# Kernel tuning notes

Hardware: AMD Instinct MI355X
Metric: run time of the kernel (lower is better)

## Reference

```python
import jax, jax.numpy as jnp
import numpy as np

# ---- config (matches init_kwargs) ----
SPATIAL_SCALE = 0.0625
POOLED = 7
OUT_DIM = 256
SAMPLE_PER_PART = 4
TRANS_STD = 0.1
PART_SIZE = 7
DEFORM_FC_DIM = 1024
# group_size == 1 -> position-sensitive group index is always 0, channel c == ctop


def _deform_roi_pool(feat, rois, offset, no_trans):
    """Faithful JAX port of DeformablePSROIPoolForward (DCNv2), group_size=1.
    feat: (B,C,H,W), rois: (N,5)=[b,x1,y1,x2,y2], offset: (N,2,P,P) or None.
    Returns (N,C,P,P)."""
    B, C, H, W = feat.shape
    N = rois.shape[0]
    P, S = POOLED, SAMPLE_PER_PART
    dt = feat.dtype
    featT = jnp.transpose(feat, (0, 2, 3, 1))  # (B,H,W,C) for spatial gathers

    b = rois[:, 0].astype(jnp.int32)
    rsw = jnp.round(rois[:, 1]) * SPATIAL_SCALE - 0.5
    rsh = jnp.round(rois[:, 2]) * SPATIAL_SCALE - 0.5
    rew = (jnp.round(rois[:, 3]) + 1.0) * SPATIAL_SCALE - 0.5
    reh = (jnp.round(rois[:, 4]) + 1.0) * SPATIAL_SCALE - 0.5
    roi_w = jnp.maximum(rew - rsw, 0.1)
    roi_h = jnp.maximum(reh - rsh, 0.1)
    bin_h = roi_h / P            # (N,)
    bin_w = roi_w / P
    sub_h = bin_h / S
    sub_w = bin_w / S

    ph = jnp.arange(P)
    pw = jnp.arange(P)
    part_h = jnp.floor(ph.astype(dt) / P * PART_SIZE).astype(jnp.int32)  # == ph when part_size==P
    part_w = jnp.floor(pw.astype(dt) / P * PART_SIZE).astype(jnp.int32)

    if no_trans:
        tx = jnp.zeros((N, P, P), dt)
        ty = jnp.zeros((N, P, P), dt)
    else:
        tx = offset[:, 0][:, part_h][:, :, part_w] * TRANS_STD  # (N,P,P)
        ty = offset[:, 1][:, part_h][:, :, part_w] * TRANS_STD

    hstart = ph.astype(dt)[None, :, None] * bin_h[:, None, None] + rsh[:, None, None] + ty * roi_h[:, None, None]
    wstart = pw.astype(dt)[None, None, :] * bin_w[:, None, None] + rsw[:, None, None] + tx * roi_w[:, None, None]

    ih = jnp.arange(S).astype(dt)
    iw = jnp.arange(S).astype(dt)
    # sample coords, shape (N,P,P,S,S); ih along axis -2, iw along axis -1
    h = hstart[..., None, None] + ih[:, None] * sub_h[:, None, None, None, None]
    w = wstart[..., None, None] + iw[None, :] * sub_w[:, None, None, None, None]

    valid = (w >= -0.5) & (w <= W - 0.5) & (h >= -0.5) & (h <= H - 0.5)
    hc = jnp.clip(h, 0.0, H - 1.0)
    wc = jnp.clip(w, 0.0, W - 1.0)
    h0 = jnp.floor(hc).astype(jnp.int32)
    w0 = jnp.floor(wc).astype(jnp.int32)
    h1 = jnp.minimum(h0 + 1, H - 1)
    w1 = jnp.minimum(w0 + 1, W - 1)
    lh = hc - h0.astype(dt)
    lw = wc - w0.astype(dt)

    bidx = b[:, None, None, None, None]

    def g(yy, xx):  # (N,P,P,S,S,C)
        return featT[bidx, yy, xx]

    val = (g(h0, w0) * ((1 - lh) * (1 - lw))[..., None]
           + g(h0, w1) * ((1 - lh) * lw)[..., None]
           + g(h1, w0) * (lh * (1 - lw))[..., None]
           + g(h1, w1) * (lh * lw)[..., None])
    val = jnp.where(valid[..., None], val, jnp.zeros((), dt))
    ssum = val.sum(axis=(3, 4))                       # (N,P,P,C)
    cnt = valid.sum(axis=(3, 4)).astype(dt)           # (N,P,P)
    out = jnp.where(cnt[..., None] > 0, ssum / jnp.maximum(cnt, 1.0)[..., None], jnp.zeros((), dt))
    return jnp.transpose(out, (0, 3, 1, 2))           # (N,C,P,P)


def setup_inputs() -> dict:
    key = jax.random.key(0)
    ks = jax.random.split(key, 12)
    B, C, H, W = 2, OUT_DIM, 100, 100
    N = 512
    img = H / SPATIAL_SCALE  # 1600

    feat = jax.random.normal(ks[0], (B, C, H, W), jnp.float32)

    bi = jax.random.randint(ks[1], (N,), 0, B).astype(jnp.float32)
    x1 = jax.random.uniform(ks[2], (N,), jnp.float32, 0.0, img - 420.0)
    y1 = jax.random.uniform(ks[3], (N,), jnp.float32, 0.0, img - 420.0)
    x2 = x1 + jax.random.uniform(ks[4], (N,), jnp.float32, 32.0, 400.0)
    y2 = y1 + jax.random.uniform(ks[5], (N,), jnp.float32, 32.0, 400.0)
    rois = jnp.stack([bi, x1, y1, x2, y2], axis=1)

    fin = POOLED * POOLED * OUT_DIM  # 12544
    w1 = jax.random.normal(ks[6], (DEFORM_FC_DIM, fin), jnp.float32) / np.sqrt(fin)
    b1 = jnp.zeros((DEFORM_FC_DIM,), jnp.float32)
    w2 = jax.random.normal(ks[7], (DEFORM_FC_DIM, DEFORM_FC_DIM), jnp.float32) / np.sqrt(DEFORM_FC_DIM)
    b2 = jnp.zeros((DEFORM_FC_DIM,), jnp.float32)
    # original init zeroes the last layer; use small random so offsets/mask are non-trivial
    w3 = jax.random.normal(ks[8], (POOLED * POOLED * 3, DEFORM_FC_DIM), jnp.float32) * 0.01
    b3 = jnp.zeros((POOLED * POOLED * 3,), jnp.float32)
    return {"input": feat, "rois": rois, "w1": w1, "b1": b1, "w2": w2, "b2": b2, "w3": w3, "b3": b3}


def reference(input, rois, w1, b1, w2, b2, w3, b3):
    N = rois.shape[0]
    P = POOLED
    # pass 1: plain (no_trans) deformable RoI pooling to predict offsets/mask
    roi0 = _deform_roi_pool(input, rois, None, no_trans=True)      # (N,C,P,P)
    x = roi0.reshape(N, -1)
    x = jax.nn.relu(x @ w1.T + b1)
    x = jax.nn.relu(x @ w2.T + b2)
    om = (x @ w3.T + b3).reshape(N, 3, P, P)
    offset = om[:, 0:2]                                            # (N,2,P,P) [trans_x, trans_y]
    mask = jax.nn.sigmoid(om[:, 2:3])                              # (N,1,P,P)
    # pass 2: deformable pooling with learned offsets, modulated by mask
    out = _deform_roi_pool(input, rois, offset, no_trans=False) * mask
    return out
```

## Files before the change

kernel.cpp:

```cpp
#include <hip/hip_runtime.h>

#define BB 2
#define CC 256
#define HH 100
#define WW 100
#define NROI 512
#define KDIM 12544
#define FC 1024

typedef _Float16 half_t;
typedef _Float16 f16x2 __attribute__((ext_vector_type(2)));
typedef _Float16 f16x8 __attribute__((ext_vector_type(8)));
typedef _Float16 f16x4 __attribute__((ext_vector_type(4)));
typedef float f32x4 __attribute__((ext_vector_type(4)));

__device__ __forceinline__ void gload16(const half_t* g, half_t* l) {
  __builtin_amdgcn_global_load_lds(
      (const __attribute__((address_space(1))) unsigned int*)g,
      (__attribute__((address_space(3))) unsigned int*)l, 16, 0, 0);
}

__global__ __launch_bounds__(256) void prep(const float* __restrict__ feat,
                                            half_t* __restrict__ featT,
                                            const float* __restrict__ w1,
                                            half_t* __restrict__ w1h,
                                            const float* __restrict__ w2,
                                            half_t* __restrict__ w2h) {
  int bid = blockIdx.x;
  if (bid < 12544) {
    int i4 = (bid * 256 + threadIdx.x) * 4;
    float4 v = *(const float4*)(w1 + i4);
    f16x4 o;
    o[0] = (half_t)v.x; o[1] = (half_t)v.y; o[2] = (half_t)v.z; o[3] = (half_t)v.w;
    *(f16x4*)(w1h + i4) = o;
    return;
  }
  bid -= 12544;
  if (bid < 1024) {
    int i4 = (bid * 256 + threadIdx.x) * 4;
    float4 v = *(const float4*)(w2 + i4);
    f16x4 o;
    o[0] = (half_t)v.x; o[1] = (half_t)v.y; o[2] = (half_t)v.z; o[3] = (half_t)v.w;
    *(f16x4*)(w2h + i4) = o;
    return;
  }
  bid -= 1024;
  __shared__ float tile[32][33];
  const int bx = bid % 313;
  const int rem = bid / 313;
  const int by = rem & 7;
  const int bz = rem >> 3;
  const int tx = threadIdx.x & 31, ty = threadIdx.x >> 5;
  const int hw0 = bx * 32;
  const int c0 = by * 32;
  const float* fb = feat + (size_t)bz * CC * (HH * WW);
#pragma unroll
  for (int i = 0; i < 4; i++) {
    int c = c0 + ty + i * 8;
    int hw = hw0 + tx;
    tile[ty + i * 8][tx] = (hw < HH * WW) ? fb[(size_t)c * (HH * WW) + hw] : 0.0f;
  }
  __syncthreads();
  half_t* ob = featT + (size_t)bz * (HH * WW) * CC;
#pragma unroll
  for (int i = 0; i < 4; i++) {
    int hw = hw0 + ty + i * 8;
    int c = c0 + tx;
    if (hw < HH * WW) ob[(size_t)hw * CC + c] = (half_t)tile[tx][ty + i * 8];
  }
}

struct PixW { int idx; float w; };

template <bool PASS2>
__global__ __launch_bounds__(512) void pool_kernel(const half_t* __restrict__ featT,
                                                   const float* __restrict__ rois,
                                                   const float* __restrict__ part3,
                                                   const float* __restrict__ b3,
                                                   half_t* __restrict__ xout,
                                                   float* __restrict__ out) {
  __shared__ __align__(16) PixW s_pix[49 * 32];
  __shared__ int s_cnt[49];
  __shared__ float s_scale[49];
  __shared__ float  s_outf[PASS2 ? KDIM : 1];
  __shared__ half_t s_outh[PASS2 ? 1 : KDIM];

  const int n = blockIdx.x;
  const int tid = threadIdx.x;
  const float* r = rois + n * 5;
  const int b = (int)r[0];
  const float rsw = rintf(r[1]) * 0.0625f - 0.5f;
  const float rsh = rintf(r[2]) * 0.0625f - 0.5f;
  const float rew = (rintf(r[3]) + 1.0f) * 0.0625f - 0.5f;
  const float reh = (rintf(r[4]) + 1.0f) * 0.0625f - 0.5f;
  const float roi_w = fmaxf(rew - rsw, 0.1f);
  const float roi_h = fmaxf(reh - rsh, 0.1f);
  const float bin_h = roi_h / 7.0f, bin_w = roi_w / 7.0f;
  const float sub_h = bin_h * 0.25f, sub_w = bin_w * 0.25f;
  const half_t* fb = featT + (size_t)b * (HH * WW) * CC;

  if (tid < 49) {
    const int p = tid, ph = p / 7, pw = p - ph * 7;
    float tx = 0.0f, ty = 0.0f, mask = 1.0f;
    if (PASS2) {
      float o0 = b3[p], o1 = b3[49 + p], o2 = b3[98 + p];
#pragma unroll
      for (int zz = 0; zz < 8; zz++) {
        const float* pz = part3 + ((size_t)zz * NROI + n) * 147;
        o0 += pz[p]; o1 += pz[49 + p]; o2 += pz[98 + p];
      }
      tx = o0 * 0.1f;
      ty = o1 * 0.1f;
      mask = 1.0f / (1.0f + expf(-o2));
    }
    const float hst = (float)ph * bin_h + rsh + ty * roi_h;
    const float wst = (float)pw * bin_w + rsw + tx * roi_w;
    float wh[6] = {0, 0, 0, 0, 0, 0};
    float hc0 = fminf(fmaxf(hst, 0.0f), 99.0f);
    const int r0 = (int)hc0;
    int rtop = r0;
    float vsh = 0.0f;
#pragma unroll
    for (int i = 0; i < 4; i++) {
      float h = hst + (float)i * sub_h;
      bool v = (h >= -0.5f) && (h <= (float)HH - 0.5f);
      float hc = fminf(fmaxf(h, 0.0f), 99.0f);
      int h0 = (int)hc;
      float lh = hc - (float)h0;
      int h1 = min(h0 + 1, HH - 1);
      if (v) { wh[h0 - r0] += 1.0f - lh; wh[h1 - r0] += lh; vsh += 1.0f; }
      rtop = h1;
    }
    float wwc[6] = {0, 0, 0, 0, 0, 0};
    float wc0 = fminf(fmaxf(wst, 0.0f), 99.0f);
    const int c0 = (int)wc0;
    int ctop = c0;
    float vsw = 0.0f;
#pragma unroll
    for (int j = 0; j < 4; j++) {
      float w = wst + (float)j * sub_w;
      bool v = (w >= -0.5f) && (w <= (float)WW - 0.5f);
      float wc = fminf(fmaxf(w, 0.0f), 99.0f);
      int w0 = (int)wc;
      float lw = wc - (float)w0;
      int w1 = min(w0 + 1, WW - 1);
      if (v) { wwc[w0 - c0] += 1.0f - lw; wwc[w1 - c0] += lw; vsw += 1.0f; }
      ctop = w1;
    }
    const int nr = rtop - r0 + 1, nc = ctop - c0 + 1;
    float cntf = vsh * vsw;
    s_scale[p] = (cntf > 0.0f) ? mask / cntf : 0.0f;
    PixW* dst = &s_pix[p * 32];
    int m = 0;
    for (int ri = 0; ri < nr; ri++) {
      int rowoff = (r0 + ri) * WW + c0;
      for (int ci = 0; ci < nc; ci++) {
        dst[m].idx = (rowoff + ci) * CC;
        dst[m].w = wh[ri] * wwc[ci];
        m++;
      }
    }
    while (m & 7) { dst[m].idx = 0; dst[m].w = 0.0f; m++; }
    s_cnt[p] = m;
  }
  __syncthreads();

  const int wv = tid >> 6;
  const int lane = tid & 63;
  const int half = lane >> 5;
  const int c8 = (lane & 31) * 8;
  for (int p = wv; p < 49; p += 8) {
    const int cnt = s_cnt[p];
    const PixW* cp = &s_pix[p * 32];
    float a0 = 0, a1 = 0, a2 = 0, a3 = 0, a4 = 0, a5 = 0, a6 = 0, a7 = 0;
    for (int q = 0; q < cnt; q += 8) {
      PixW e0 = cp[q + 0 + half];
      PixW e1 = cp[q + 2 + half];
      PixW e2 = cp[q + 4 + half];
      PixW e3 = cp[q + 6 + half];
      f16x8 v0 = *(const f16x8*)(fb + e0.idx + c8);
      f16x8 v1 = *(const f16x8*)(fb + e1.idx + c8);
      f16x8 v2 = *(const f16x8*)(fb + e2.idx + c8);
      f16x8 v3 = *(const f16x8*)(fb + e3.idx + c8);
      a0 += e0.w * (float)v0[0] + e1.w * (float)v1[0] + e2.w * (float)v2[0] + e3.w * (float)v3[0];
      a1 += e0.w * (float)v0[1] + e1.w * (float)v1[1] + e2.w * (float)v2[1] + e3.w * (float)v3[1];
      a2 += e0.w * (float)v0[2] + e1.w * (float)v1[2] + e2.w * (float)v2[2] + e3.w * (float)v3[2];
      a3 += e0.w * (float)v0[3] + e1.w * (float)v1[3] + e2.w * (float)v2[3] + e3.w * (float)v3[3];
      a4 += e0.w * (float)v0[4] + e1.w * (float)v1[4] + e2.w * (float)v2[4] + e3.w * (float)v3[4];
      a5 += e0.w * (float)v0[5] + e1.w * (float)v1[5] + e2.w * (float)v2[5] + e3.w * (float)v3[5];
      a6 += e0.w * (float)v0[6] + e1.w * (float)v1[6] + e2.w * (float)v2[6] + e3.w * (float)v3[6];
      a7 += e0.w * (float)v0[7] + e1.w * (float)v1[7] + e2.w * (float)v2[7] + e3.w * (float)v3[7];
    }
    a0 += __shfl_xor(a0, 32); a1 += __shfl_xor(a1, 32);
    a2 += __shfl_xor(a2, 32); a3 += __shfl_xor(a3, 32);
    a4 += __shfl_xor(a4, 32); a5 += __shfl_xor(a5, 32);
    a6 += __shfl_xor(a6, 32); a7 += __shfl_xor(a7, 32);
    if (half == 0) {
      float sc = s_scale[p];
      a0 *= sc; a1 *= sc; a2 *= sc; a3 *= sc; a4 *= sc; a5 *= sc; a6 *= sc; a7 *= sc;
      if (PASS2) {
        s_outf[(c8 + 0) * 49 + p] = a0;
        s_outf[(c8 + 1) * 49 + p] = a1;
        s_outf[(c8 + 2) * 49 + p] = a2;
        s_outf[(c8 + 3) * 49 + p] = a3;
        s_outf[(c8 + 4) * 49 + p] = a4;
        s_outf[(c8 + 5) * 49 + p] = a5;
        s_outf[(c8 + 6) * 49 + p] = a6;
        s_outf[(c8 + 7) * 49 + p] = a7;
      } else {
        s_outh[(c8 + 0) * 49 + p] = (half_t)a0;
        s_outh[(c8 + 1) * 49 + p] = (half_t)a1;
        s_outh[(c8 + 2) * 49 + p] = (half_t)a2;
        s_outh[(c8 + 3) * 49 + p] = (half_t)a3;
        s_outh[(c8 + 4) * 49 + p] = (half_t)a4;
        s_outh[(c8 + 5) * 49 + p] = (half_t)a5;
        s_outh[(c8 + 6) * 49 + p] = (half_t)a6;
        s_outh[(c8 + 7) * 49 + p] = (half_t)a7;
      }
    }
  }
  __syncthreads();

  if (PASS2) {
    float* ob = out + (size_t)n * KDIM;
    for (int l = tid * 4; l < KDIM; l += 2048)
      *(float4*)(ob + l) = *(const float4*)(s_outf + l);
  } else {
    half_t* ob = xout + (size_t)n * KDIM;
    for (int l = tid * 8; l < KDIM; l += 4096)
      *(f16x8*)(ob + l) = *(const f16x8*)(s_outh + l);
  }
}

template <int SK>
__global__ __launch_bounds__(256, 2) void gemm_lds(const half_t* __restrict__ A,
                                                   const half_t* __restrict__ B,
                                                   float* __restrict__ P, int K) {
  __shared__ half_t As[2][128 * 64];
  __shared__ half_t Bs[2][128 * 64];
  const int d = blockIdx.x + gridDim.x * (blockIdx.y + gridDim.y * blockIdx.z);
  const int g = (d & 7) * (SK * 4) + (d >> 3);
  const int z = g >> 5;
  const int tile = g & 31;
  const int m0 = (tile & 3) * 128;
  const int n0 = (tile >> 2) * 128;
  const int Kc = K / SK;
  const int kbeg = z * Kc;
  const int tid = threadIdx.x;
  const int lane = tid & 63;
  const int wave = tid >> 6;
  const int wm = (wave & 1) * 64;
  const int wn = (wave >> 1) * 64;
  const int fr = lane & 15;
  const int kc0 = lane >> 4;
  const int lr = lane >> 3;
  const int lc = (lane & 7) ^ lr;
  const half_t* Ag = A + (size_t)(m0 + wave * 8 + lr) * K + kbeg + lc * 8;
  const half_t* Bg = B + (size_t)(n0 + wave * 8 + lr) * K + kbeg + lc * 8;
  f32x4 acc[4][4] = {};

  auto stage = [&](int buf, int ko) {
#pragma unroll
    for (int s = 0; s < 4; s++)
      gload16(Ag + (size_t)(32 * s) * K + ko, &As[buf][s * 2048 + wave * 512]);
#pragma unroll
    for (int s = 0; s < 4; s++)
      gload16(Bg + (size_t)(32 * s) * K + ko, &Bs[buf][s * 2048 + wave * 512]);
  };

  const int iters = Kc >> 6;
  stage(0, 0);
  if (iters > 1) {
    stage(1, 64);
    asm volatile("s_waitcnt vmcnt(8)" ::: "memory");
  } else {
    asm volatile("s_waitcnt vmcnt(0)" ::: "memory");
  }
  __builtin_amdgcn_s_barrier();

  for (int it = 0; it < iters; it++) {
    const int cur = it & 1;
#pragma unroll
    for (int ks = 0; ks < 2; ks++) {
      const int swz = ((kc0 + ks * 4) ^ (fr & 7)) * 8;
      f16x8 af[4], bf[4];
#pragma unroll
      for (int i = 0; i < 4; i++) af[i] = *(const f16x8*)&As[cur][(wm + i * 16 + fr) * 64 + swz];
#pragma unroll
      for (int j = 0; j < 4; j++) bf[j] = *(const f16x8*)&Bs[cur][(wn + j * 16 + fr) * 64 + swz];
      __builtin_amdgcn_s_setprio(1);
#pragma unroll
      for (int i = 0; i < 4; i++)
#pragma unroll
        for (int j = 0; j < 4; j++)
          acc[i][j] = __builtin_amdgcn_mfma_f32_16x16x32_f16(af[i], bf[j], acc[i][j], 0, 0, 0);
      __builtin_amdgcn_s_setprio(0);
    }
    asm volatile("s_waitcnt lgkmcnt(0)" ::: "memory");
    __builtin_amdgcn_s_barrier();
    const bool issue = (it + 2 < iters);
    if (issue) stage(cur, (it + 2) * 64);
    if (it + 1 < iters) {
      if (issue) asm volatile("s_waitcnt vmcnt(8)" ::: "memory");
      else       asm volatile("s_waitcnt vmcnt(0)" ::: "memory");
      __builtin_amdgcn_s_barrier();
    }
  }
  float* Pz = P + (((size_t)z * 32 + tile) * 4 + wave) * 4096;
#pragma unroll
  for (int i = 0; i < 4; i++)
#pragma unroll
    for (int j = 0; j < 4; j++)
#pragma unroll
      for (int rr = 0; rr < 4; rr++)
        Pz[((i * 4 + j) * 4 + rr) * 64 + lane] = acc[i][j][rr];
}

template <bool OUT16, bool RELU, int SK>
__global__ __launch_bounds__(256) void reduce_blocked(const float* __restrict__ P,
                                                      const float* __restrict__ bias,
                                                      void* __restrict__ out,
                                                      int MN, int N) {
  int i4 = (blockIdx.x * 256 + threadIdx.x) * 4;
  if (i4 >= MN) return;
  float4 s = *(const float4*)(P + i4);
#pragma unroll
  for (int z = 1; z < SK; z++) {
    float4 t = *(const float4*)(P + (size_t)z * MN + i4);
    s.x += t.x; s.y += t.y; s.z += t.z; s.w += t.w;
  }
  const int lane0 = i4 & 63;
  const int q     = (i4 >> 6) & 63;
  const int wave  = (i4 >> 12) & 3;
  const int bx    = (i4 >> 14) & 3;
  const int by    = (i4 >> 16) & 7;
  const int rr = q & 3, j_ = (q >> 2) & 3, i_ = q >> 4;
  const int row = bx * 128 + (wave & 1) * 64 + i_ * 16 + (lane0 >> 4) * 4 + rr;
  const int col = by * 128 + (wave >> 1) * 64 + j_ * 16 + (lane0 & 15);
  float4 bv = *(const float4*)(bias + col);
  s.x += bv.x; s.y += bv.y; s.z += bv.z; s.w += bv.w;
  if (RELU) {
    s.x = fmaxf(s.x, 0.0f); s.y = fmaxf(s.y, 0.0f);
    s.z = fmaxf(s.z, 0.0f); s.w = fmaxf(s.w, 0.0f);
  }
  size_t o = (size_t)row * N + col;
  if (OUT16) {
    f16x4 ov;
    ov[0] = (half_t)s.x; ov[1] = (half_t)s.y; ov[2] = (half_t)s.z; ov[3] = (half_t)s.w;
    *(f16x4*)((half_t*)out + o) = ov;
  } else {
    *(float4*)((float*)out + o) = s;
  }
}

__global__ __launch_bounds__(192) void gemm3_part(const float* __restrict__ h2,
                                                  const float* __restrict__ w3,
                                                  float* __restrict__ part3) {
  __shared__ float hs[8][128];
  const int n0 = blockIdx.x * 8;
  const int z = blockIdx.y;
  const int tid = threadIdx.x;
  for (int idx = tid; idx < 1024; idx += 192) {
    int nn = idx >> 7, kk = idx & 127;
    hs[nn][kk] = h2[(size_t)(n0 + nn) * FC + z * 128 + kk];
  }
  __syncthreads();
  const int j = tid;
  if (j < 147) {
    const float* wr = w3 + (size_t)j * FC + z * 128;
    float acc[8] = {0, 0, 0, 0, 0, 0, 0, 0};
    for (int k = 0; k < 128; k += 4) {
      float4 wv = *(const float4*)(wr + k);
#pragma unroll
      for (int nn = 0; nn < 8; nn++)
        acc[nn] += hs[nn][k] * wv.x + hs[nn][k + 1] * wv.y +
                   hs[nn][k + 2] * wv.z + hs[nn][k + 3] * wv.w;
    }
#pragma unroll
    for (int nn = 0; nn < 8; nn++)
      part3[((size_t)z * NROI + n0 + nn) * 147 + j] = acc[nn];
  }
}

extern "C" void kernel_launch(void* const* d_in, const int* in_sizes, int n_in,
                              void* d_out, int out_size, void* d_ws, size_t ws_size,
                              hipStream_t stream) {
  const float* feat = (const float*)d_in[0];
  const float* rois = (const float*)d_in[1];
  const float* w1 = (const float*)d_in[2];
  const float* b1 = (const float*)d_in[3];
  const float* w2 = (const float*)d_in[4];
  const float* b2 = (const float*)d_in[5];
  const float* w3 = (const float*)d_in[6];
  const float* b3 = (const float*)d_in[7];
  float* out = (float*)d_out;
  char* ws = (char*)d_ws;

  half_t* featT = (half_t*)ws;
  half_t* xh    = (half_t*)(ws + 10240000);
  half_t* w1h   = (half_t*)(ws + 23085056);
  half_t* w2h   = (half_t*)(ws + 48775168);
  half_t* h1    = (half_t*)(ws + 50872320);
  float*  h2    = (float*)(ws + 51920896);
  float*  part  = (float*)(ws + 54319104);

  const int MN = NROI * FC;

  prep<<<dim3(18576), dim3(256), 0, stream>>>(feat, featT, w1, w1h, w2, w2h);
  pool_kernel<false><<<dim3(NROI), dim3(512), 0, stream>>>(featT, rois, nullptr, nullptr, xh, nullptr);

  gemm_lds<14><<<dim3(4, 8, 14), dim3(256), 0, stream>>>(xh, w1h, part, KDIM);
  reduce_blocked<true, true, 14><<<dim3(MN / 1024), dim3(256), 0, stream>>>(part, b1, (void*)h1, MN, FC);

  gemm_lds<8><<<dim3(4, 8, 8), dim3(256), 0, stream>>>(h1, w2h, part, FC);
  reduce_blocked<false, true, 8><<<dim3(MN / 1024), dim3(256), 0, stream>>>(part, b2, (void*)h2, MN, FC);

  gemm3_part<<<dim3(64, 8), dim3(192), 0, stream>>>(h2, w3, part);
  pool_kernel<true><<<dim3(NROI), dim3(512), 0, stream>>>(featT, rois, part, b3, nullptr, out);
}
```

Measured before the change: 220.3 us.

## Widen GEMM1 tiles, fuse GEMM2 reduce into GEMM3, unroll pooling gathers

GEMM1 moves to a 512-thread kernel with 256x128 tiles, which halves the tile count and reuses each B tile across more rows; its reduce kernel gets a matching index map. The separate GEMM2 split-K reduce is removed: the third GEMM now sums the eight partial slices, adds the bias and applies ReLU while loading its input tile. The pooling gather loop is unrolled to 16 entries, with padding raised to 16, so more loads are in flight. The cost is fewer blocks per GEMM1 wave, extra zero-weight padding gathers, and more register pressure.

```diff
diff --git a/kernel.cpp b/kernel.cpp
--- a/kernel.cpp
+++ b/kernel.cpp
@@ -160,7 +160,7 @@
         m++;
       }
     }
-    while (m & 7) { dst[m].idx = 0; dst[m].w = 0.0f; m++; }
+    while (m & 15) { dst[m].idx = 0; dst[m].w = 0.0f; m++; }
     s_cnt[p] = m;
   }
   __syncthreads();
@@ -173,23 +173,39 @@
     const int cnt = s_cnt[p];
     const PixW* cp = &s_pix[p * 32];
     float a0 = 0, a1 = 0, a2 = 0, a3 = 0, a4 = 0, a5 = 0, a6 = 0, a7 = 0;
-    for (int q = 0; q < cnt; q += 8) {
+    for (int q = 0; q < cnt; q += 16) {
       PixW e0 = cp[q + 0 + half];
       PixW e1 = cp[q + 2 + half];
       PixW e2 = cp[q + 4 + half];
       PixW e3 = cp[q + 6 + half];
+      PixW e4 = cp[q + 8 + half];
+      PixW e5 = cp[q + 10 + half];
+      PixW e6 = cp[q + 12 + half];
+      PixW e7 = cp[q + 14 + half];
       f16x8 v0 = *(const f16x8*)(fb + e0.idx + c8);
       f16x8 v1 = *(const f16x8*)(fb + e1.idx + c8);
       f16x8 v2 = *(const f16x8*)(fb + e2.idx + c8);
       f16x8 v3 = *(const f16x8*)(fb + e3.idx + c8);
-      a0 += e0.w * (float)v0[0] + e1.w * (float)v1[0] + e2.w * (float)v2[0] + e3.w * (float)v3[0];
-      a1 += e0.w * (float)v0[1] + e1.w * (float)v1[1] + e2.w * (float)v2[1] + e3.w * (float)v3[1];
-      a2 += e0.w * (float)v0[2] + e1.w * (float)v1[2] + e2.w * (float)v2[2] + e3.w * (float)v3[2];
-      a3 += e0.w * (float)v0[3] + e1.w * (float)v1[3] + e2.w * (float)v2[3] + e3.w * (float)v3[3];
-      a4 += e0.w * (float)v0[4] + e1.w * (float)v1[4] + e2.w * (float)v2[4] + e3.w * (float)v3[4];
-      a5 += e0.w * (float)v0[5] + e1.w * (float)v1[5] + e2.w * (float)v2[5] + e3.w * (float)v3[5];
-      a6 += e0.w * (float)v0[6] + e1.w * (float)v1[6] + e2.w * (float)v2[6] + e3.w * (float)v3[6];
-      a7 += e0.w * (float)v0[7] + e1.w * (float)v1[7] + e2.w * (float)v2[7] + e3.w * (float)v3[7];
+      f16x8 v4 = *(const f16x8*)(fb + e4.idx + c8);
+      f16x8 v5 = *(const f16x8*)(fb + e5.idx + c8);
+      f16x8 v6 = *(const f16x8*)(fb + e6.idx + c8);
+      f16x8 v7 = *(const f16x8*)(fb + e7.idx + c8);
+      a0 += e0.w * (float)v0[0] + e1.w * (float)v1[0] + e2.w * (float)v2[0] + e3.w * (float)v3[0]
+          + e4.w * (float)v4[0] + e5.w * (float)v5[0] + e6.w * (float)v6[0] + e7.w * (float)v7[0];
+      a1 += e0.w * (float)v0[1] + e1.w * (float)v1[1] + e2.w * (float)v2[1] + e3.w * (float)v3[1]
+          + e4.w * (float)v4[1] + e5.w * (float)v5[1] + e6.w * (float)v6[1] + e7.w * (float)v7[1];
+      a2 += e0.w * (float)v0[2] + e1.w * (float)v1[2] + e2.w * (float)v2[2] + e3.w * (float)v3[2]
+          + e4.w * (float)v4[2] + e5.w * (float)v5[2] + e6.w * (float)v6[2] + e7.w * (float)v7[2];
+      a3 += e0.w * (float)v0[3] + e1.w * (float)v1[3] + e2.w * (float)v2[3] + e3.w * (float)v3[3]
+          + e4.w * (float)v4[3] + e5.w * (float)v5[3] + e6.w * (float)v6[3] + e7.w * (float)v7[3];
+      a4 += e0.w * (float)v0[4] + e1.w * (float)v1[4] + e2.w * (float)v2[4] + e3.w * (float)v3[4]
+          + e4.w * (float)v4[4] + e5.w * (float)v5[4] + e6.w * (float)v6[4] + e7.w * (float)v7[4];
+      a5 += e0.w * (float)v0[5] + e1.w * (float)v1[5] + e2.w * (float)v2[5] + e3.w * (float)v3[5]
+          + e4.w * (float)v4[5] + e5.w * (float)v5[5] + e6.w * (float)v6[5] + e7.w * (float)v7[5];
+      a6 += e0.w * (float)v0[6] + e1.w * (float)v1[6] + e2.w * (float)v2[6] + e3.w * (float)v3[6]
+          + e4.w * (float)v4[6] + e5.w * (float)v5[6] + e6.w * (float)v6[6] + e7.w * (float)v7[6];
+      a7 += e0.w * (float)v0[7] + e1.w * (float)v1[7] + e2.w * (float)v2[7] + e3.w * (float)v3[7]
+          + e4.w * (float)v4[7] + e5.w * (float)v5[7] + e6.w * (float)v6[7] + e7.w * (float)v7[7];
     }
     a0 += __shfl_xor(a0, 32); a1 += __shfl_xor(a1, 32);
     a2 += __shfl_xor(a2, 32); a3 += __shfl_xor(a3, 32);
@@ -233,6 +249,126 @@
 }
 
 template <int SK>
+__global__ __launch_bounds__(512, 1) void gemm_lds_w(const half_t* __restrict__ A,
+                                                     const half_t* __restrict__ B,
+                                                     float* __restrict__ P, int K) {
+  __shared__ half_t As[2][256 * 64];
+  __shared__ half_t Bs[2][128 * 64];
+  const int d = blockIdx.x + gridDim.x * (blockIdx.y + gridDim.y * blockIdx.z);
+  const int g = (d & 7) * (SK * 2) + (d >> 3);
+  const int z = g >> 4;
+  const int tile = g & 15;
+  const int m0 = (tile & 1) * 256;
+  const int n0 = (tile >> 1) * 128;
+  const int Kc = K / SK;
+  const int kbeg = z * Kc;
+  const int tid = threadIdx.x;
+  const int lane = tid & 63;
+  const int wave = tid >> 6;
+  const int wm = (wave & 3) * 64;
+  const int wn = (wave >> 2) * 64;
+  const int fr = lane & 15;
+  const int kc0 = lane >> 4;
+  const int lr = lane >> 3;
+  const int lc = (lane & 7) ^ lr;
+  const half_t* Ag = A + (size_t)(m0 + wave * 32 + lr) * K + kbeg + lc * 8;
+  const half_t* Bg = B + (size_t)(n0 + wave * 16 + lr) * K + kbeg + lc * 8;
+  f32x4 acc[4][4] = {};
+
+  auto stage = [&](int buf, int ko) {
+#pragma unroll
+    for (int s = 0; s < 4; s++)
+      gload16(Ag + (size_t)(8 * s) * K + ko, &As[buf][wave * 2048 + s * 512]);
+#pragma unroll
+    for (int s = 0; s < 2; s++)
+      gload16(Bg + (size_t)(8 * s) * K + ko, &Bs[buf][wave * 1024 + s * 512]);
+  };
+
+  const int iters = Kc >> 6;
+  stage(0, 0);
+  if (iters > 1) {
+    stage(1, 64);
+    asm volatile("s_waitcnt vmcnt(6)" ::: "memory");
+  } else {
+    asm volatile("s_waitcnt vmcnt(0)" ::: "memory");
+  }
+  __builtin_amdgcn_s_barrier();
+
+  for (int it = 0; it < iters; it++) {
+    const int cur = it & 1;
+#pragma unroll
+    for (int ks = 0; ks < 2; ks++) {
+      const int swz = ((kc0 + ks * 4) ^ (fr & 7)) * 8;
+      f16x8 af[4], bf[4];
+#pragma unroll
+      for (int i = 0; i < 4; i++) af[i] = *(const f16x8*)&As[cur][(wm + i * 16 + fr) * 64 + swz];
+#pragma unroll
+      for (int j = 0; j < 4; j++) bf[j] = *(const f16x8*)&Bs[cur][(wn + j * 16 + fr) * 64 + swz];
+      __builtin_amdgcn_s_setprio(1);
+#pragma unroll
+      for (int i = 0; i < 4; i++)
+#pragma unroll
+        for (int j = 0; j < 4; j++)
+          acc[i][j] = __builtin_amdgcn_mfma_f32_16x16x32_f16(af[i], bf[j], acc[i][j], 0, 0, 0);
+      __builtin_amdgcn_s_setprio(0);
+    }
+    asm volatile("s_waitcnt lgkmcnt(0)" ::: "memory");
+    __builtin_amdgcn_s_barrier();
+    const bool issue = (it + 2 < iters);
+    if (issue) stage(cur, (it + 2) * 64);
+    if (it + 1 < iters) {
+      if (issue) asm volatile("s_waitcnt vmcnt(6)" ::: "memory");
+      else       asm volatile("s_waitcnt vmcnt(0)" ::: "memory");
+      __builtin_amdgcn_s_barrier();
+    }
+  }
+  float* Pz = P + (((size_t)z * 16 + tile) * 8 + wave) * 4096;
+#pragma unroll
+  for (int i = 0; i < 4; i++)
+#pragma unroll
+    for (int j = 0; j < 4; j++)
+#pragma unroll
+      for (int rr = 0; rr < 4; rr++)
+        Pz[((i * 4 + j) * 4 + rr) * 64 + lane] = acc[i][j][rr];
+}
+
+template <bool OUT16, bool RELU, int SK>
+__global__ __launch_bounds__(256) void reduce_w(const float* __restrict__ P,
+                                                const float* __restrict__ bias,
+                                                void* __restrict__ out,
+                                                int MN, int N) {
+  int i4 = (blockIdx.x * 256 + threadIdx.x) * 4;
+  if (i4 >= MN) return;
+  float4 s = *(const float4*)(P + i4);
+#pragma unroll
+  for (int z = 1; z < SK; z++) {
+    float4 t = *(const float4*)(P + (size_t)z * MN + i4);
+    s.x += t.x; s.y += t.y; s.z += t.z; s.w += t.w;
+  }
+  const int lane0 = i4 & 63;
+  const int q     = (i4 >> 6) & 63;
+  const int wave  = (i4 >> 12) & 7;
+  const int tile  = (i4 >> 15) & 15;
+  const int rr = q & 3, j_ = (q >> 2) & 3, i_ = q >> 4;
+  const int row = (tile & 1) * 256 + (wave & 3) * 64 + i_ * 16 + (lane0 >> 4) * 4 + rr;
+  const int col = (tile >> 1) * 128 + (wave >> 2) * 64 + j_ * 16 + (lane0 & 15);
+  float4 bv = *(const float4*)(bias + col);
+  s.x += bv.x; s.y += bv.y; s.z += bv.z; s.w += bv.w;
+  if (RELU) {
+    s.x = fmaxf(s.x, 0.0f); s.y = fmaxf(s.y, 0.0f);
+    s.z = fmaxf(s.z, 0.0f); s.w = fmaxf(s.w, 0.0f);
+  }
+  size_t o = (size_t)row * N + col;
+  if (OUT16) {
+    f16x4 ov;
+    ov[0] = (half_t)s.x; ov[1] = (half_t)s.y; ov[2] = (half_t)s.z; ov[3] = (half_t)s.w;
+    *(f16x4*)((half_t*)out + o) = ov;
+  } else {
+    *(float4*)((float*)out + o) = s;
+  }
+}
+
+template <int SK>
 __global__ __launch_bounds__(256, 2) void gemm_lds(const half_t* __restrict__ A,
                                                    const half_t* __restrict__ B,
                                                    float* __restrict__ P, int K) {
@@ -316,58 +452,45 @@
         Pz[((i * 4 + j) * 4 + rr) * 64 + lane] = acc[i][j][rr];
 }
 
-template <bool OUT16, bool RELU, int SK>
-__global__ __launch_bounds__(256) void reduce_blocked(const float* __restrict__ P,
-                                                      const float* __restrict__ bias,
-                                                      void* __restrict__ out,
-                                                      int MN, int N) {
-  int i4 = (blockIdx.x * 256 + threadIdx.x) * 4;
-  if (i4 >= MN) return;
-  float4 s = *(const float4*)(P + i4);
-#pragma unroll
-  for (int z = 1; z < SK; z++) {
-    float4 t = *(const float4*)(P + (size_t)z * MN + i4);
-    s.x += t.x; s.y += t.y; s.z += t.z; s.w += t.w;
-  }
-  const int lane0 = i4 & 63;
-  const int q     = (i4 >> 6) & 63;
-  const int wave  = (i4 >> 12) & 3;
-  const int bx    = (i4 >> 14) & 3;
-  const int by    = (i4 >> 16) & 7;
-  const int rr = q & 3, j_ = (q >> 2) & 3, i_ = q >> 4;
-  const int row = bx * 128 + (wave & 1) * 64 + i_ * 16 + (lane0 >> 4) * 4 + rr;
-  const int col = by * 128 + (wave >> 1) * 64 + j_ * 16 + (lane0 & 15);
-  float4 bv = *(const float4*)(bias + col);
-  s.x += bv.x; s.y += bv.y; s.z += bv.z; s.w += bv.w;
-  if (RELU) {
-    s.x = fmaxf(s.x, 0.0f); s.y = fmaxf(s.y, 0.0f);
-    s.z = fmaxf(s.z, 0.0f); s.w = fmaxf(s.w, 0.0f);
-  }
-  size_t o = (size_t)row * N + col;
-  if (OUT16) {
-    f16x4 ov;
-    ov[0] = (half_t)s.x; ov[1] = (half_t)s.y; ov[2] = (half_t)s.z; ov[3] = (half_t)s.w;
-    *(f16x4*)((half_t*)out + o) = ov;
-  } else {
-    *(float4*)((float*)out + o) = s;
-  }
-}
-
-__global__ __launch_bounds__(192) void gemm3_part(const float* __restrict__ h2,
-                                                  const float* __restrict__ w3,
-                                                  float* __restrict__ part3) {
+__global__ __launch_bounds__(256) void gemm3_fused(const float* __restrict__ part2,
+                                                   const float* __restrict__ b2,
+                                                   const float* __restrict__ w3,
+                                                   float* __restrict__ part3) {
   __shared__ float hs[8][128];
   const int n0 = blockIdx.x * 8;
-  const int z = blockIdx.y;
+  const int z3 = blockIdx.y;
   const int tid = threadIdx.x;
-  for (int idx = tid; idx < 1024; idx += 192) {
-    int nn = idx >> 7, kk = idx & 127;
-    hs[nn][kk] = h2[(size_t)(n0 + nn) * FC + z * 128 + kk];
+  const int MN = NROI * FC;
+  {
+    const int idx4 = tid * 4;
+    const int nn = idx4 >> 7;
+    const int kk = idx4 & 127;
+    const int row = n0 + nn;
+    const int col = z3 * 128 + kk;
+    const int bx = (row >> 7) & 3;
+    const int by = (col >> 7) & 7;
+    const int wv = ((row >> 6) & 1) | (((col >> 6) & 1) << 1);
+    const int q  = ((row >> 4) & 3) * 16 + ((col >> 4) & 3) * 4 + (row & 3);
+    const int l0 = ((row >> 2) & 3) * 16 + (col & 15);
+    const int tile = by * 4 + bx;
+    const size_t base = (size_t)((tile * 4 + wv) * 4096 + q * 64 + l0);
+    float4 s = *(const float4*)(part2 + base);
+#pragma unroll
+    for (int z2 = 1; z2 < 8; z2++) {
+      float4 t = *(const float4*)(part2 + (size_t)z2 * MN + base);
+      s.x += t.x; s.y += t.y; s.z += t.z; s.w += t.w;
+    }
+    float4 bv = *(const float4*)(b2 + col);
+    s.x = fmaxf(s.x + bv.x, 0.0f);
+    s.y = fmaxf(s.y + bv.y, 0.0f);
+    s.z = fmaxf(s.z + bv.z, 0.0f);
+    s.w = fmaxf(s.w + bv.w, 0.0f);
+    *(float4*)(&hs[nn][kk]) = s;
   }
   __syncthreads();
   const int j = tid;
   if (j < 147) {
-    const float* wr = w3 + (size_t)j * FC + z * 128;
+    const float* wr = w3 + (size_t)j * FC + z3 * 128;
     float acc[8] = {0, 0, 0, 0, 0, 0, 0, 0};
     for (int k = 0; k < 128; k += 4) {
       float4 wv = *(const float4*)(wr + k);
@@ -378,7 +501,7 @@
     }
 #pragma unroll
     for (int nn = 0; nn < 8; nn++)
-      part3[((size_t)z * NROI + n0 + nn) * 147 + j] = acc[nn];
+      part3[((size_t)z3 * NROI + n0 + nn) * 147 + j] = acc[nn];
   }
 }
 
@@ -401,20 +524,19 @@
   half_t* w1h   = (half_t*)(ws + 23085056);
   half_t* w2h   = (half_t*)(ws + 48775168);
   half_t* h1    = (half_t*)(ws + 50872320);
-  float*  h2    = (float*)(ws + 51920896);
   float*  part  = (float*)(ws + 54319104);
+  float*  part3 = (float*)(ws + 83679232);
 
   const int MN = NROI * FC;
 
   prep<<<dim3(18576), dim3(256), 0, stream>>>(feat, featT, w1, w1h, w2, w2h);
   pool_kernel<false><<<dim3(NROI), dim3(512), 0, stream>>>(featT, rois, nullptr, nullptr, xh, nullptr);
 
-  gemm_lds<14><<<dim3(4, 8, 14), dim3(256), 0, stream>>>(xh, w1h, part, KDIM);
-  reduce_blocked<true, true, 14><<<dim3(MN / 1024), dim3(256), 0, stream>>>(part, b1, (void*)h1, MN, FC);
+  gemm_lds_w<14><<<dim3(2, 8, 14), dim3(512), 0, stream>>>(xh, w1h, part, KDIM);
+  reduce_w<true, true, 14><<<dim3(MN / 1024), dim3(256), 0, stream>>>(part, b1, (void*)h1, MN, FC);
 
   gemm_lds<8><<<dim3(4, 8, 8), dim3(256), 0, stream>>>(h1, w2h, part, FC);
-  reduce_blocked<false, true, 8><<<dim3(MN / 1024), dim3(256), 0, stream>>>(part, b2, (void*)h2, MN, FC);
-
-  gemm3_part<<<dim3(64, 8), dim3(192), 0, stream>>>(h2, w3, part);
-  pool_kernel<true><<<dim3(NROI), dim3(512), 0, stream>>>(featT, rois, part, b3, nullptr, out);
-}
+
+  gemm3_fused<<<dim3(64, 8), dim3(256), 0, stream>>>(part, b2, w3, part3);
+  pool_kernel<true><<<dim3(NROI), dim3(512), 0, stream>>>(featT, rois, part3, b3, nullptr, out);
+}
```

Result: no change. 221.8 us (+0.7%).
